# Performance work log

Measured on AMD Instinct MI355X. Metric: run time of the kernel, lower is better.

Reference implementation:

```python
import jax, jax.numpy as jnp
import numpy as np

NUM_STEPS = 10  # fixed-step Dopri5 over [0, T], dt = T/NUM_STEPS (dt0=0.1, T=1.0 in source)
B, D, H = 8192, 64, 256


def setup_inputs() -> dict:
    key = jax.random.key(0)
    ks = jax.random.split(key, 4)
    x = jax.random.normal(ks[0], (B, D), jnp.float32)
    logdet_init = jnp.zeros((B,), jnp.float32)

    def lin(k, out_dim, in_dim):
        kw, kb = jax.random.split(k)
        lim = 1.0 / np.sqrt(in_dim)
        W = jax.random.uniform(kw, (out_dim, in_dim), jnp.float32, -lim, lim)
        b = jax.random.uniform(kb, (out_dim,), jnp.float32, -lim, lim)
        return W, b

    W1, b1 = lin(ks[1], H, D)
    W2, b2 = lin(ks[2], H, H)
    W3, b3 = lin(ks[3], D, H)
    T = jnp.array(1.0, jnp.float32)
    return dict(x=x, logdet_init=logdet_init, W1=W1, b1=b1, W2=W2, b2=b2, W3=W3, b3=b3, T=T)


def reference(x, logdet_init, W1, b1, W2, b2, W3, b3, T):
    # odefunc: softplus MLP, per-sample (eqx Linear semantics: W @ y + b)
    def mlp(y):  # y: (D,)
        h = jax.nn.softplus(W1 @ y + b1)
        h = jax.nn.softplus(W2 @ h + b2)
        return W3 @ h + b3

    trace_fn = jax.vmap(lambda y: jnp.trace(jax.jacfwd(mlp)(y)))  # exact trace, [B]

    def dyn(y):  # y: [B, D] -> (dy/dt [B,D], dlogdet/dt [B])
        h = jax.nn.softplus(y @ W1.T + b1)
        h = jax.nn.softplus(h @ W2.T + b2)
        dy = h @ W3.T + b3
        return dy, trace_fn(y)

    dt = T / NUM_STEPS
    # Dormand-Prince 5(4) tableau (6 stages used for the 5th-order update)
    a21 = 1/5
    a31, a32 = 3/40, 9/40
    a41, a42, a43 = 44/45, -56/15, 32/9
    a51, a52, a53, a54 = 19372/6561, -25360/2187, 64448/6561, -212/729
    a61, a62, a63, a64, a65 = 9017/3168, -355/33, 46732/5247, 49/176, -5103/18656
    c1, c3, c4, c5, c6 = 35/384, 500/1113, 125/192, -2187/6784, 11/84

    def step(carry, _):
        y, ld = carry
        k1y, k1l = dyn(y)
        k2y, k2l = dyn(y + dt * (a21 * k1y))
        k3y, k3l = dyn(y + dt * (a31 * k1y + a32 * k2y))
        k4y, k4l = dyn(y + dt * (a41 * k1y + a42 * k2y + a43 * k3y))
        k5y, k5l = dyn(y + dt * (a51 * k1y + a52 * k2y + a53 * k3y + a54 * k4y))
        k6y, k6l = dyn(y + dt * (a61 * k1y + a62 * k2y + a63 * k3y + a64 * k4y + a65 * k5y))
        y_new = y + dt * (c1 * k1y + c3 * k3y + c4 * k4y + c5 * k5y + c6 * k6y)
        ld_new = ld + dt * (c1 * k1l + c3 * k3l + c4 * k4l + c5 * k5l + c6 * k6l)
        return (y_new, ld_new), None

    (y_f, ld_f), _ = jax.lax.scan(step, (x, logdet_init), None, length=NUM_STEPS)
    return (y_f, ld_f)
```

## Files before the change

### kernel.cpp

```cpp
#include <hip/hip_runtime.h>

typedef __attribute__((ext_vector_type(4))) float f32x4;
typedef __attribute__((ext_vector_type(8))) short bf16x8;
typedef __attribute__((ext_vector_type(4))) short bf16x4;

#define MFMA16(a, b, c) __builtin_amdgcn_mfma_f32_16x16x32_bf16(a, b, c, 0, 0, 0)

#define W1F_OFF 0
#define W2F_OFF 16384
#define CF_OFF  81920
#define W3F_OFF 147456

__device__ __forceinline__ short f2bf(float f) {
  unsigned u = __builtin_bit_cast(unsigned, f);
  u += 0x7FFFu + ((u >> 16) & 1u);
  return (short)(u >> 16);
}

__device__ __forceinline__ void sp_sig(float z, float& h, float& s) {
  float t = __expf(-fabsf(z));
#if __has_builtin(__builtin_amdgcn_rcpf)
  float r = __builtin_amdgcn_rcpf(1.f + t);
#else
  float r = 1.f / (1.f + t);
#endif
  h = fmaxf(z, 0.f) + __logf(1.f + t);
  s = (z >= 0.f) ? r : 1.f - r;
}

__global__ __launch_bounds__(512) void cnf_prep(const float* __restrict__ W1,
                                                const float* __restrict__ W2,
                                                const float* __restrict__ W3,
                                                short* __restrict__ ws) {
  int e = blockIdx.x * 512 + threadIdx.x;
  int j = e & 7;
  int l = (e >> 3) & 63;
  int g = l >> 4, lm = l & 15;
  float val;
  if (e < 16384) {
    int t = e >> 9, kt = t & 1, mt = t >> 1;
    val = W1[(mt * 16 + lm) * 64 + kt * 32 + g * 8 + j];
  } else if (e < 81920) {
    int t = (e - 16384) >> 9, kt = t & 7, mt = t >> 3;
    val = W2[(mt * 16 + lm) * 256 + kt * 32 + g * 8 + j];
  } else if (e < 147456) {
    int t = (e - 81920) >> 9, kt = t & 7, mt = t >> 3;
    int m = mt * 16 + lm, k = kt * 32 + g * 8 + j;
    float a2 = 0.f;
#pragma unroll 16
    for (int d = 0; d < 64; ++d) a2 += W1[k * 64 + d] * W3[d * 256 + m];
    val = W2[m * 256 + k] * a2;
  } else {
    int t = (e - 147456) >> 9, kt = t & 7, mt = t >> 3;
    val = W3[(mt * 16 + lm) * 256 + kt * 32 + g * 8 + j];
  }
  ws[e] = f2bf(val);
}

__global__ __launch_bounds__(512) void cnf_main(
    const float* __restrict__ x, const float* __restrict__ ld_init,
    const float* __restrict__ b1g, const float* __restrict__ b2g,
    const float* __restrict__ b3g, const float* __restrict__ Tg,
    const short* __restrict__ ws, float* __restrict__ outy,
    float* __restrict__ outl) {
  __shared__ __align__(16) short w1f[16384];
  __shared__ __align__(16) short w3f[16384];
  __shared__ __align__(16) short ytL[32 * 88];
  __shared__ __align__(16) short h1L[32 * 264];
  __shared__ __align__(16) short s1L_[32 * 264];
  __shared__ __align__(16) short h2L[32 * 264];
  __shared__ __align__(16) float dyL[32 * 68];
  __shared__ float trP[8][32];
  __shared__ float b1L[256], b2L[256], b3L[64];

  const int tid = threadIdx.x;
  const int lane = tid & 63, wv = tid >> 6;
  const int sl = tid >> 4, q = tid & 15;
  const int lg = lane >> 4, lm = lane & 15;
  const int ko8 = lg << 3;

  {
    const f32x4* s1p = (const f32x4*)ws;
    f32x4* d1 = (f32x4*)w1f;
#pragma unroll
    for (int i = 0; i < 4; ++i) d1[tid + 512 * i] = s1p[tid + 512 * i];
    const f32x4* s3p = (const f32x4*)(ws + W3F_OFF);
    f32x4* d3 = (f32x4*)w3f;
#pragma unroll
    for (int i = 0; i < 4; ++i) d3[tid + 512 * i] = s3p[tid + 512 * i];
    if (tid < 256) { b1L[tid] = b1g[tid]; b2L[tid] = b2g[tid]; }
    else if (tid < 320) b3L[tid - 256] = b3g[tid - 256];
  }

  const bf16x8* w2fG = (const bf16x8*)(ws + W2F_OFF);
  const bf16x8* cfG  = (const bf16x8*)(ws + CF_OFF);

  const int sg = blockIdx.x * 32 + sl;
  f32x4 y = *(const f32x4*)&x[sg * 64 + q * 4];
  float ld = ld_init[sg];
  const float dt = Tg[0] * 0.1f;

  __syncthreads();

  auto dyn = [&](f32x4 yin, f32x4& dy, float& tr) {
    bf16x4 yb;
#pragma unroll
    for (int r = 0; r < 4; ++r) yb[r] = f2bf(yin[r]);
    *(bf16x4*)&ytL[sl * 88 + q * 4] = yb;
    __syncthreads();

    f32x4 a00 = {0,0,0,0}, a01 = {0,0,0,0}, a10 = {0,0,0,0}, a11 = {0,0,0,0};
#pragma unroll
    for (int kt = 0; kt < 2; ++kt) {
      bf16x8 A0 = *(const bf16x8*)&w1f[(((2 * wv + 0) * 2 + kt) * 64 + lane) * 8];
      bf16x8 A1 = *(const bf16x8*)&w1f[(((2 * wv + 1) * 2 + kt) * 64 + lane) * 8];
      bf16x8 B0 = *(const bf16x8*)&ytL[lm * 88 + kt * 32 + ko8];
      bf16x8 B1 = *(const bf16x8*)&ytL[(16 + lm) * 88 + kt * 32 + ko8];
      a00 = MFMA16(A0, B0, a00); a01 = MFMA16(A0, B1, a01);
      a10 = MFMA16(A1, B0, a10); a11 = MFMA16(A1, B1, a11);
    }
    {
      auto epi1 = [&](f32x4 z4, int r2, int c) {
        int row0 = (2 * wv + r2) * 16 + (lg << 2);
        int sc = c * 16 + lm;
        bf16x4 hh, ss;
#pragma unroll
        for (int r = 0; r < 4; ++r) {
          float h, s;
          sp_sig(z4[r] + b1L[row0 + r], h, s);
          hh[r] = f2bf(h); ss[r] = f2bf(s);
        }
        *(bf16x4*)&h1L[sc * 264 + row0] = hh;
        *(bf16x4*)&s1L_[sc * 264 + row0] = ss;
      };
      epi1(a00, 0, 0); epi1(a01, 0, 1); epi1(a10, 1, 0); epi1(a11, 1, 1);
    }
    __syncthreads();

    f32x4 c00 = {0,0,0,0}, c01 = {0,0,0,0}, c10 = {0,0,0,0}, c11 = {0,0,0,0};
#pragma unroll
    for (int kt = 0; kt < 8; ++kt) {
      bf16x8 A0 = w2fG[((2 * wv + 0) * 8 + kt) * 64 + lane];
      bf16x8 A1 = w2fG[((2 * wv + 1) * 8 + kt) * 64 + lane];
      bf16x8 B0 = *(const bf16x8*)&h1L[lm * 264 + kt * 32 + ko8];
      bf16x8 B1 = *(const bf16x8*)&h1L[(16 + lm) * 264 + kt * 32 + ko8];
      c00 = MFMA16(A0, B0, c00); c01 = MFMA16(A0, B1, c01);
      c10 = MFMA16(A1, B0, c10); c11 = MFMA16(A1, B1, c11);
    }
    f32x4 s200, s201, s210, s211;
    {
      auto epi2 = [&](f32x4 z4, int r2, int c, f32x4& s2o) {
        int row0 = (2 * wv + r2) * 16 + (lg << 2);
        int sc = c * 16 + lm;
        bf16x4 hh;
#pragma unroll
        for (int r = 0; r < 4; ++r) {
          float h, s;
          sp_sig(z4[r] + b2L[row0 + r], h, s);
          hh[r] = f2bf(h); s2o[r] = s;
        }
        *(bf16x4*)&h2L[sc * 264 + row0] = hh;
      };
      epi2(c00, 0, 0, s200); epi2(c01, 0, 1, s201);
      epi2(c10, 1, 0, s210); epi2(c11, 1, 1, s211);
    }
    __syncthreads();

    f32x4 u00 = {0,0,0,0}, u01 = {0,0,0,0}, u10 = {0,0,0,0}, u11 = {0,0,0,0};
#pragma unroll
    for (int kt = 0; kt < 8; ++kt) {
      bf16x8 A0 = cfG[((2 * wv + 0) * 8 + kt) * 64 + lane];
      bf16x8 A1 = cfG[((2 * wv + 1) * 8 + kt) * 64 + lane];
      bf16x8 B0 = *(const bf16x8*)&s1L_[lm * 264 + kt * 32 + ko8];
      bf16x8 B1 = *(const bf16x8*)&s1L_[(16 + lm) * 264 + kt * 32 + ko8];
      u00 = MFMA16(A0, B0, u00); u01 = MFMA16(A0, B1, u01);
      u10 = MFMA16(A1, B0, u10); u11 = MFMA16(A1, B1, u11);
    }
    float pl0 = 0.f, pl1 = 0.f;
#pragma unroll
    for (int r = 0; r < 4; ++r) {
      pl0 += u00[r] * s200[r] + u10[r] * s210[r];
      pl1 += u01[r] * s201[r] + u11[r] * s211[r];
    }
    pl0 += __shfl_xor(pl0, 16); pl0 += __shfl_xor(pl0, 32);
    pl1 += __shfl_xor(pl1, 16); pl1 += __shfl_xor(pl1, 32);
    if (lane < 16) { trP[wv][lane] = pl0; trP[wv][16 + lane] = pl1; }

    f32x4 d3a = {0,0,0,0};
    const int m3 = wv & 3, c3 = wv >> 2;
#pragma unroll
    for (int kt = 0; kt < 8; ++kt) {
      bf16x8 A0 = *(const bf16x8*)&w3f[((m3 * 8 + kt) * 64 + lane) * 8];
      bf16x8 B0 = *(const bf16x8*)&h2L[(c3 * 16 + lm) * 264 + kt * 32 + ko8];
      d3a = MFMA16(A0, B0, d3a);
    }
    {
      int d0r = m3 * 16 + (lg << 2);
      int sc = c3 * 16 + lm;
      f32x4 dv;
#pragma unroll
      for (int r = 0; r < 4; ++r) dv[r] = d3a[r] + b3L[d0r + r];
      *(f32x4*)&dyL[sc * 68 + d0r] = dv;
    }
    __syncthreads();

    dy = *(const f32x4*)&dyL[sl * 68 + q * 4];
    float t = 0.f;
#pragma unroll
    for (int w = 0; w < 8; ++w) t += trP[w][sl];
    tr = t;
  };

  const float A21 = 1.f / 5.f;
  const float A31 = 3.f / 40.f, A32 = 9.f / 40.f;
  const float A41 = 44.f / 45.f, A42 = -56.f / 15.f, A43 = 32.f / 9.f;
  const float A51 = 19372.f / 6561.f, A52 = -25360.f / 2187.f,
              A53 = 64448.f / 6561.f, A54 = -212.f / 729.f;
  const float A61 = 9017.f / 3168.f, A62 = -355.f / 33.f,
              A63 = 46732.f / 5247.f, A64 = 49.f / 176.f, A65 = -5103.f / 18656.f;
  const float C1 = 35.f / 384.f, C3 = 500.f / 1113.f, C4 = 125.f / 192.f,
              C5 = -2187.f / 6784.f, C6 = 11.f / 84.f;

  f32x4 k1, k2, k3, k4, k5, k6;
  float l1, l2, l3, l4, l5, l6;
#pragma unroll 1
  for (int step = 0; step < 10; ++step) {
    dyn(y, k1, l1);
    dyn(y + dt * (A21 * k1), k2, l2);
    dyn(y + dt * (A31 * k1 + A32 * k2), k3, l3);
    dyn(y + dt * (A41 * k1 + A42 * k2 + A43 * k3), k4, l4);
    dyn(y + dt * (A51 * k1 + A52 * k2 + A53 * k3 + A54 * k4), k5, l5);
    dyn(y + dt * (A61 * k1 + A62 * k2 + A63 * k3 + A64 * k4 + A65 * k5), k6, l6);
    y = y + dt * (C1 * k1 + C3 * k3 + C4 * k4 + C5 * k5 + C6 * k6);
    ld = ld + dt * (C1 * l1 + C3 * l3 + C4 * l4 + C5 * l5 + C6 * l6);
  }

  *(f32x4*)&outy[sg * 64 + q * 4] = y;
  if (q == 0) outl[sg] = ld;
}

extern "C" void kernel_launch(void* const* d_in, const int* in_sizes, int n_in,
                              void* d_out, int out_size, void* d_ws, size_t ws_size,
                              hipStream_t stream) {
  const float* x  = (const float*)d_in[0];
  const float* l0 = (const float*)d_in[1];
  const float* W1 = (const float*)d_in[2];
  const float* b1 = (const float*)d_in[3];
  const float* W2 = (const float*)d_in[4];
  const float* b2 = (const float*)d_in[5];
  const float* W3 = (const float*)d_in[6];
  const float* b3 = (const float*)d_in[7];
  const float* Tp = (const float*)d_in[8];
  short* ws = (short*)d_ws;

  cnf_prep<<<dim3(320), dim3(512), 0, stream>>>(W1, W2, W3, ws);

  float* outy = (float*)d_out;
  float* outl = outy + 8192 * 64;
  cnf_main<<<dim3(256), dim3(512), 0, stream>>>(x, l0, b1, b2, b3, Tp, ws, outy, outl);
}
```

Before: 317.5 us.

## Double block to 16 waves and split per-wave MFMA tiles, cheapen softplus

Doubles the workgroup size to 1024 threads so each of 16 waves owns one 16-row M-tile instead of two. The W3 GEMM is split over K halves, with the partial sums reduced through shared memory. Biases are folded into the MFMA accumulator initial values, and one barrier between layer 2 and the trace GEMM is dropped. Softplus and sigmoid now use exp2/log2 intrinsics with packed bf16 conversion, and dt is folded into the RK coefficients. The aim is more latency hiding per CU and less epilogue ALU work, at the cost of higher register pressure under the 1024-thread bound and an extra dy reduction.

After: 536.7 us. 69.0% more time.

```diff
diff --git a/kernel.cpp b/kernel.cpp
--- a/kernel.cpp
+++ b/kernel.cpp
@@ -1,8 +1,9 @@
 #include <hip/hip_runtime.h>
 
+typedef __attribute__((ext_vector_type(2))) float f32x2;
 typedef __attribute__((ext_vector_type(4))) float f32x4;
 typedef __attribute__((ext_vector_type(8))) short bf16x8;
-typedef __attribute__((ext_vector_type(4))) short bf16x4;
+typedef __attribute__((ext_vector_type(2))) unsigned u32x2;
 
 #define MFMA16(a, b, c) __builtin_amdgcn_mfma_f32_16x16x32_bf16(a, b, c, 0, 0, 0)
 
@@ -17,15 +18,40 @@
   return (short)(u >> 16);
 }
 
+__device__ __forceinline__ unsigned cvt_pk_bf16(float lo, float hi) {
+  unsigned r;
+  asm("v_cvt_pk_bf16_f32 %0, %1, %2" : "=v"(r) : "v"(lo), "v"(hi));
+  return r;
+}
+
 __device__ __forceinline__ void sp_sig(float z, float& h, float& s) {
-  float t = __expf(-fabsf(z));
+  float a = fabsf(z);
+#if __has_builtin(__builtin_amdgcn_exp2f)
+  float t = __builtin_amdgcn_exp2f(a * -1.44269504f);
+#else
+  float t = __expf(-a);
+#endif
+  float o = 1.f + t;
 #if __has_builtin(__builtin_amdgcn_rcpf)
-  float r = __builtin_amdgcn_rcpf(1.f + t);
+  float r = __builtin_amdgcn_rcpf(o);
 #else
-  float r = 1.f / (1.f + t);
+  float r = 1.f / o;
 #endif
-  h = fmaxf(z, 0.f) + __logf(1.f + t);
+#if __has_builtin(__builtin_amdgcn_logf)
+  float l2 = __builtin_amdgcn_logf(o);
+#else
+  float l2 = __logf(o) * 1.44269504f;
+#endif
+  h = fmaxf(z, 0.f) + 0.69314718f * l2;
   s = (z >= 0.f) ? r : 1.f - r;
+}
+
+__device__ __forceinline__ void sp_sig4(const f32x4& z, u32x2& hp, f32x4& sv) {
+  float h0, h1, h2, h3, s0, s1, s2, s3;
+  sp_sig(z[0], h0, s0); sp_sig(z[1], h1, s1);
+  sp_sig(z[2], h2, s2); sp_sig(z[3], h3, s3);
+  hp[0] = cvt_pk_bf16(h0, h1); hp[1] = cvt_pk_bf16(h2, h3);
+  sv[0] = s0; sv[1] = s1; sv[2] = s2; sv[3] = s3;
 }
 
 __global__ __launch_bounds__(512) void cnf_prep(const float* __restrict__ W1,
@@ -57,7 +83,7 @@
   ws[e] = f2bf(val);
 }
 
-__global__ __launch_bounds__(512) void cnf_main(
+__global__ __launch_bounds__(1024) void cnf_main(
     const float* __restrict__ x, const float* __restrict__ ld_init,
     const float* __restrict__ b1g, const float* __restrict__ b2g,
     const float* __restrict__ b3g, const float* __restrict__ Tg,
@@ -69,174 +95,149 @@
   __shared__ __align__(16) short h1L[32 * 264];
   __shared__ __align__(16) short s1L_[32 * 264];
   __shared__ __align__(16) short h2L[32 * 264];
-  __shared__ __align__(16) float dyL[32 * 68];
-  __shared__ float trP[8][32];
-  __shared__ float b1L[256], b2L[256], b3L[64];
+  __shared__ __align__(16) float dyL[2][32][68];
+  __shared__ __align__(16) float trPT[32][16];
 
   const int tid = threadIdx.x;
   const int lane = tid & 63, wv = tid >> 6;
-  const int sl = tid >> 4, q = tid & 15;
+  const int sl = tid >> 5, q2 = tid & 31;
   const int lg = lane >> 4, lm = lane & 15;
   const int ko8 = lg << 3;
 
   {
-    const f32x4* s1p = (const f32x4*)ws;
+    const f32x4* s1p = (const f32x4*)(ws + W1F_OFF);
     f32x4* d1 = (f32x4*)w1f;
-#pragma unroll
-    for (int i = 0; i < 4; ++i) d1[tid + 512 * i] = s1p[tid + 512 * i];
+    d1[tid] = s1p[tid]; d1[tid + 1024] = s1p[tid + 1024];
     const f32x4* s3p = (const f32x4*)(ws + W3F_OFF);
     f32x4* d3 = (f32x4*)w3f;
-#pragma unroll
-    for (int i = 0; i < 4; ++i) d3[tid + 512 * i] = s3p[tid + 512 * i];
-    if (tid < 256) { b1L[tid] = b1g[tid]; b2L[tid] = b2g[tid]; }
-    else if (tid < 320) b3L[tid - 256] = b3g[tid - 256];
+    d3[tid] = s3p[tid]; d3[tid + 1024] = s3p[tid + 1024];
   }
+
+  const int row0 = wv * 16 + (lg << 2);
+  const f32x4 bias1 = *(const f32x4*)&b1g[row0];
+  const f32x4 bias2 = *(const f32x4*)&b2g[row0];
+  const int m3 = wv & 3, c3 = (wv >> 2) & 1, kh = wv >> 3;
+  f32x4 bias3 = {0.f, 0.f, 0.f, 0.f};
+  if (kh == 0) bias3 = *(const f32x4*)&b3g[m3 * 16 + (lg << 2)];
 
   const bf16x8* w2fG = (const bf16x8*)(ws + W2F_OFF);
   const bf16x8* cfG  = (const bf16x8*)(ws + CF_OFF);
 
   const int sg = blockIdx.x * 32 + sl;
-  f32x4 y = *(const f32x4*)&x[sg * 64 + q * 4];
+  f32x2 y = *(const f32x2*)&x[sg * 64 + q2 * 2];
   float ld = ld_init[sg];
   const float dt = Tg[0] * 0.1f;
 
   __syncthreads();
 
-  auto dyn = [&](f32x4 yin, f32x4& dy, float& tr) {
-    bf16x4 yb;
-#pragma unroll
-    for (int r = 0; r < 4; ++r) yb[r] = f2bf(yin[r]);
-    *(bf16x4*)&ytL[sl * 88 + q * 4] = yb;
-    __syncthreads();
-
-    f32x4 a00 = {0,0,0,0}, a01 = {0,0,0,0}, a10 = {0,0,0,0}, a11 = {0,0,0,0};
+  auto dyn = [&](f32x2 yin, f32x2& dy, float& tr) {
+    *(unsigned*)&ytL[sl * 88 + q2 * 2] = cvt_pk_bf16(yin[0], yin[1]);
+    __syncthreads();
+
+    f32x4 a0 = bias1, a1 = bias1;
 #pragma unroll
     for (int kt = 0; kt < 2; ++kt) {
-      bf16x8 A0 = *(const bf16x8*)&w1f[(((2 * wv + 0) * 2 + kt) * 64 + lane) * 8];
-      bf16x8 A1 = *(const bf16x8*)&w1f[(((2 * wv + 1) * 2 + kt) * 64 + lane) * 8];
+      bf16x8 A = *(const bf16x8*)&w1f[((wv * 2 + kt) * 64 + lane) * 8];
       bf16x8 B0 = *(const bf16x8*)&ytL[lm * 88 + kt * 32 + ko8];
       bf16x8 B1 = *(const bf16x8*)&ytL[(16 + lm) * 88 + kt * 32 + ko8];
-      a00 = MFMA16(A0, B0, a00); a01 = MFMA16(A0, B1, a01);
-      a10 = MFMA16(A1, B0, a10); a11 = MFMA16(A1, B1, a11);
+      a0 = MFMA16(A, B0, a0); a1 = MFMA16(A, B1, a1);
     }
     {
-      auto epi1 = [&](f32x4 z4, int r2, int c) {
-        int row0 = (2 * wv + r2) * 16 + (lg << 2);
-        int sc = c * 16 + lm;
-        bf16x4 hh, ss;
-#pragma unroll
-        for (int r = 0; r < 4; ++r) {
-          float h, s;
-          sp_sig(z4[r] + b1L[row0 + r], h, s);
-          hh[r] = f2bf(h); ss[r] = f2bf(s);
-        }
-        *(bf16x4*)&h1L[sc * 264 + row0] = hh;
-        *(bf16x4*)&s1L_[sc * 264 + row0] = ss;
-      };
-      epi1(a00, 0, 0); epi1(a01, 0, 1); epi1(a10, 1, 0); epi1(a11, 1, 1);
-    }
-    __syncthreads();
-
-    f32x4 c00 = {0,0,0,0}, c01 = {0,0,0,0}, c10 = {0,0,0,0}, c11 = {0,0,0,0};
+      u32x2 hp; f32x4 sv;
+      sp_sig4(a0, hp, sv);
+      u32x2 sp0 = {cvt_pk_bf16(sv[0], sv[1]), cvt_pk_bf16(sv[2], sv[3])};
+      *(u32x2*)&h1L[lm * 264 + row0] = hp;
+      *(u32x2*)&s1L_[lm * 264 + row0] = sp0;
+      sp_sig4(a1, hp, sv);
+      u32x2 sp1 = {cvt_pk_bf16(sv[0], sv[1]), cvt_pk_bf16(sv[2], sv[3])};
+      *(u32x2*)&h1L[(16 + lm) * 264 + row0] = hp;
+      *(u32x2*)&s1L_[(16 + lm) * 264 + row0] = sp1;
+    }
+    __syncthreads();
+
+    f32x4 c0 = bias2, c1 = bias2;
 #pragma unroll
     for (int kt = 0; kt < 8; ++kt) {
-      bf16x8 A0 = w2fG[((2 * wv + 0) * 8 + kt) * 64 + lane];
-      bf16x8 A1 = w2fG[((2 * wv + 1) * 8 + kt) * 64 + lane];
+      bf16x8 A = w2fG[(wv * 8 + kt) * 64 + lane];
       bf16x8 B0 = *(const bf16x8*)&h1L[lm * 264 + kt * 32 + ko8];
       bf16x8 B1 = *(const bf16x8*)&h1L[(16 + lm) * 264 + kt * 32 + ko8];
-      c00 = MFMA16(A0, B0, c00); c01 = MFMA16(A0, B1, c01);
-      c10 = MFMA16(A1, B0, c10); c11 = MFMA16(A1, B1, c11);
-    }
-    f32x4 s200, s201, s210, s211;
+      c0 = MFMA16(A, B0, c0); c1 = MFMA16(A, B1, c1);
+    }
+    f32x4 s20, s21;
     {
-      auto epi2 = [&](f32x4 z4, int r2, int c, f32x4& s2o) {
-        int row0 = (2 * wv + r2) * 16 + (lg << 2);
-        int sc = c * 16 + lm;
-        bf16x4 hh;
-#pragma unroll
-        for (int r = 0; r < 4; ++r) {
-          float h, s;
-          sp_sig(z4[r] + b2L[row0 + r], h, s);
-          hh[r] = f2bf(h); s2o[r] = s;
-        }
-        *(bf16x4*)&h2L[sc * 264 + row0] = hh;
-      };
-      epi2(c00, 0, 0, s200); epi2(c01, 0, 1, s201);
-      epi2(c10, 1, 0, s210); epi2(c11, 1, 1, s211);
-    }
-    __syncthreads();
-
-    f32x4 u00 = {0,0,0,0}, u01 = {0,0,0,0}, u10 = {0,0,0,0}, u11 = {0,0,0,0};
+      u32x2 hp;
+      sp_sig4(c0, hp, s20);
+      *(u32x2*)&h2L[lm * 264 + row0] = hp;
+      sp_sig4(c1, hp, s21);
+      *(u32x2*)&h2L[(16 + lm) * 264 + row0] = hp;
+    }
+
+    f32x4 u0 = {0.f, 0.f, 0.f, 0.f}, u1 = {0.f, 0.f, 0.f, 0.f};
 #pragma unroll
     for (int kt = 0; kt < 8; ++kt) {
-      bf16x8 A0 = cfG[((2 * wv + 0) * 8 + kt) * 64 + lane];
-      bf16x8 A1 = cfG[((2 * wv + 1) * 8 + kt) * 64 + lane];
+      bf16x8 A = cfG[(wv * 8 + kt) * 64 + lane];
       bf16x8 B0 = *(const bf16x8*)&s1L_[lm * 264 + kt * 32 + ko8];
       bf16x8 B1 = *(const bf16x8*)&s1L_[(16 + lm) * 264 + kt * 32 + ko8];
-      u00 = MFMA16(A0, B0, u00); u01 = MFMA16(A0, B1, u01);
-      u10 = MFMA16(A1, B0, u10); u11 = MFMA16(A1, B1, u11);
-    }
-    float pl0 = 0.f, pl1 = 0.f;
-#pragma unroll
-    for (int r = 0; r < 4; ++r) {
-      pl0 += u00[r] * s200[r] + u10[r] * s210[r];
-      pl1 += u01[r] * s201[r] + u11[r] * s211[r];
-    }
+      u0 = MFMA16(A, B0, u0); u1 = MFMA16(A, B1, u1);
+    }
+    float pl0 = u0[0] * s20[0] + u0[1] * s20[1] + u0[2] * s20[2] + u0[3] * s20[3];
+    float pl1 = u1[0] * s21[0] + u1[1] * s21[1] + u1[2] * s21[2] + u1[3] * s21[3];
     pl0 += __shfl_xor(pl0, 16); pl0 += __shfl_xor(pl0, 32);
     pl1 += __shfl_xor(pl1, 16); pl1 += __shfl_xor(pl1, 32);
-    if (lane < 16) { trP[wv][lane] = pl0; trP[wv][16 + lane] = pl1; }
-
-    f32x4 d3a = {0,0,0,0};
-    const int m3 = wv & 3, c3 = wv >> 2;
-#pragma unroll
-    for (int kt = 0; kt < 8; ++kt) {
-      bf16x8 A0 = *(const bf16x8*)&w3f[((m3 * 8 + kt) * 64 + lane) * 8];
-      bf16x8 B0 = *(const bf16x8*)&h2L[(c3 * 16 + lm) * 264 + kt * 32 + ko8];
-      d3a = MFMA16(A0, B0, d3a);
-    }
-    {
-      int d0r = m3 * 16 + (lg << 2);
-      int sc = c3 * 16 + lm;
-      f32x4 dv;
-#pragma unroll
-      for (int r = 0; r < 4; ++r) dv[r] = d3a[r] + b3L[d0r + r];
-      *(f32x4*)&dyL[sc * 68 + d0r] = dv;
-    }
-    __syncthreads();
-
-    dy = *(const f32x4*)&dyL[sl * 68 + q * 4];
-    float t = 0.f;
-#pragma unroll
-    for (int w = 0; w < 8; ++w) t += trP[w][sl];
-    tr = t;
+    if (lane < 16) { trPT[lm][wv] = pl0; trPT[16 + lm][wv] = pl1; }
+    __syncthreads();
+
+    f32x4 d3a = bias3;
+#pragma unroll
+    for (int k = 0; k < 4; ++k) {
+      int kt = kh * 4 + k;
+      bf16x8 A = *(const bf16x8*)&w3f[((m3 * 8 + kt) * 64 + lane) * 8];
+      bf16x8 B = *(const bf16x8*)&h2L[(c3 * 16 + lm) * 264 + kt * 32 + ko8];
+      d3a = MFMA16(A, B, d3a);
+    }
+    *(f32x4*)&dyL[kh][c3 * 16 + lm][m3 * 16 + (lg << 2)] = d3a;
+    __syncthreads();
+
+    f32x2 da = *(const f32x2*)&dyL[0][sl][q2 * 2];
+    f32x2 db = *(const f32x2*)&dyL[1][sl][q2 * 2];
+    dy = da + db;
+    f32x4 t0 = *(const f32x4*)&trPT[sl][0];
+    f32x4 t1 = *(const f32x4*)&trPT[sl][4];
+    f32x4 t2 = *(const f32x4*)&trPT[sl][8];
+    f32x4 t3 = *(const f32x4*)&trPT[sl][12];
+    f32x4 ts = t0 + t1 + t2 + t3;
+    tr = ts[0] + ts[1] + ts[2] + ts[3];
   };
 
-  const float A21 = 1.f / 5.f;
-  const float A31 = 3.f / 40.f, A32 = 9.f / 40.f;
-  const float A41 = 44.f / 45.f, A42 = -56.f / 15.f, A43 = 32.f / 9.f;
-  const float A51 = 19372.f / 6561.f, A52 = -25360.f / 2187.f,
-              A53 = 64448.f / 6561.f, A54 = -212.f / 729.f;
-  const float A61 = 9017.f / 3168.f, A62 = -355.f / 33.f,
-              A63 = 46732.f / 5247.f, A64 = 49.f / 176.f, A65 = -5103.f / 18656.f;
-  const float C1 = 35.f / 384.f, C3 = 500.f / 1113.f, C4 = 125.f / 192.f,
-              C5 = -2187.f / 6784.f, C6 = 11.f / 84.f;
-
-  f32x4 k1, k2, k3, k4, k5, k6;
+  const float A21 = dt * (1.f / 5.f);
+  const float A31 = dt * (3.f / 40.f), A32 = dt * (9.f / 40.f);
+  const float A41 = dt * (44.f / 45.f), A42 = dt * (-56.f / 15.f),
+              A43 = dt * (32.f / 9.f);
+  const float A51 = dt * (19372.f / 6561.f), A52 = dt * (-25360.f / 2187.f),
+              A53 = dt * (64448.f / 6561.f), A54 = dt * (-212.f / 729.f);
+  const float A61 = dt * (9017.f / 3168.f), A62 = dt * (-355.f / 33.f),
+              A63 = dt * (46732.f / 5247.f), A64 = dt * (49.f / 176.f),
+              A65 = dt * (-5103.f / 18656.f);
+  const float C1 = dt * (35.f / 384.f), C3 = dt * (500.f / 1113.f),
+              C4 = dt * (125.f / 192.f), C5 = dt * (-2187.f / 6784.f),
+              C6 = dt * (11.f / 84.f);
+
+  f32x2 k1, k2, k3, k4, k5, k6;
   float l1, l2, l3, l4, l5, l6;
 #pragma unroll 1
   for (int step = 0; step < 10; ++step) {
     dyn(y, k1, l1);
-    dyn(y + dt * (A21 * k1), k2, l2);
-    dyn(y + dt * (A31 * k1 + A32 * k2), k3, l3);
-    dyn(y + dt * (A41 * k1 + A42 * k2 + A43 * k3), k4, l4);
-    dyn(y + dt * (A51 * k1 + A52 * k2 + A53 * k3 + A54 * k4), k5, l5);
-    dyn(y + dt * (A61 * k1 + A62 * k2 + A63 * k3 + A64 * k4 + A65 * k5), k6, l6);
-    y = y + dt * (C1 * k1 + C3 * k3 + C4 * k4 + C5 * k5 + C6 * k6);
-    ld = ld + dt * (C1 * l1 + C3 * l3 + C4 * l4 + C5 * l5 + C6 * l6);
+    dyn(y + A21 * k1, k2, l2);
+    dyn(y + A31 * k1 + A32 * k2, k3, l3);
+    dyn(y + A41 * k1 + A42 * k2 + A43 * k3, k4, l4);
+    dyn(y + A51 * k1 + A52 * k2 + A53 * k3 + A54 * k4, k5, l5);
+    dyn(y + A61 * k1 + A62 * k2 + A63 * k3 + A64 * k4 + A65 * k5, k6, l6);
+    y = y + C1 * k1 + C3 * k3 + C4 * k4 + C5 * k5 + C6 * k6;
+    ld = ld + C1 * l1 + C3 * l3 + C4 * l4 + C5 * l5 + C6 * l6;
   }
 
-  *(f32x4*)&outy[sg * 64 + q * 4] = y;
-  if (q == 0) outl[sg] = ld;
+  *(f32x2*)&outy[sg * 64 + q2 * 2] = y;
+  if (q2 == 0) outl[sg] = ld;
 }
 
 extern "C" void kernel_launch(void* const* d_in, const int* in_sizes, int n_in,
@@ -257,5 +258,6 @@
 
   float* outy = (float*)d_out;
   float* outl = outy + 8192 * 64;
-  cnf_main<<<dim3(256), dim3(512), 0, stream>>>(x, l0, b1, b2, b3, Tp, ws, outy, outl);
-}
+  cnf_main<<<dim3(256), dim3(1024), 0, stream>>>(x, l0, b1, b2, b3, Tp, ws,
+                                                 outy, outl);
+}
```
